# Optimization experiments

Hardware: AMD Instinct MI355X
Metric: run time of the kernel (lower is better)

Reference implementation:

```python
import jax, jax.numpy as jnp
import numpy as np

D_MODEL = 768
NUM_HEADS = 12
SEGMENT_LENGTHS = (2048, 4096, 8192)
DILATION_RATES = (1, 2, 4)
LN_EPS = 1e-5


def setup_inputs() -> dict:
    key = jax.random.key(0)
    ks = jax.random.split(key, 8)
    b, n, dm = 2, 8192, D_MODEL
    s = 1.0 / np.sqrt(dm)
    return {
        "x": jax.random.normal(ks[0], (b, n, dm), dtype=jnp.float32),
        "w_in": jax.random.normal(ks[1], (dm, dm), dtype=jnp.float32) * s,
        "b_in": jnp.zeros((dm,), dtype=jnp.float32),
        "w_out": jax.random.normal(ks[2], (dm, dm), dtype=jnp.float32) * s,
        "b_out": jnp.zeros((dm,), dtype=jnp.float32),
        "ln_gamma": jnp.ones((dm,), dtype=jnp.float32),
        "ln_beta": jnp.zeros((dm,), dtype=jnp.float32),
    }


def _dilated_attention(q, k, v):
    # q, k, v: (b, n, h, d)
    b, n, h, d = q.shape
    num_groups = len(DILATION_RATES)
    group_sizes = [h // num_groups] * num_groups
    for i in range(h % num_groups):
        group_sizes[i] += 1
    scale = 1.0 / jnp.sqrt(jnp.asarray(d, q.dtype))
    out = jnp.zeros_like(q)
    for i, (g, r, s) in enumerate(zip(group_sizes, DILATION_RATES, SEGMENT_LENGTHS)):
        offset = i % r
        hmin, hmax = i * g, (i + 1) * g
        nseg = n // s
        def slc(t):
            # (b, nseg, s, h, d) -> strided dilation slice + head group slice
            return t.reshape(b, nseg, s, h, d)[:, :, offset::r, hmin:hmax, :]
        qs, ks_, vs = slc(q), slc(k), slc(v)  # (b, nseg, se, g, d), se = s // r
        attn = jnp.einsum('bnqhd,bnkhd->bnhqk', qs, ks_) * scale
        attn = jax.nn.softmax(attn, axis=-1)
        x = jnp.einsum('bnhqk,bnkhd->bnqhd', attn, vs)  # (b, nseg, se, g, d)
        # renormalize by sum over (segment, within-segment) dims, as in source
        x = x / x.sum(axis=(1, 2), keepdims=True)
        out = (out.reshape(b, nseg, s, h, d)
                  .at[:, :, offset::r, hmin:hmax, :].add(x)
                  .reshape(b, n, h, d))
    return out / num_groups


def reference(x, w_in, b_in, w_out, b_out, ln_gamma, ln_beta):
    b, n, dm = x.shape
    hd = dm // NUM_HEADS
    # QKVProjectionOption.SAME: q = k = v = proj(x)
    q = x @ w_in.T + b_in
    qh = q.reshape(b, n, NUM_HEADS, hd)
    o = _dilated_attention(qh, qh, qh)
    o = o.reshape(b, n, dm)
    mu = o.mean(axis=-1, keepdims=True)
    var = ((o - mu) ** 2).mean(axis=-1, keepdims=True)
    o = (o - mu) / jnp.sqrt(var + LN_EPS) * ln_gamma + ln_beta
    return o @ w_out.T + b_out
```

## Files before the change

### kernel.cpp

```cpp
#include <hip/hip_runtime.h>
#include <hip/hip_bf16.h>
#include <math.h>

#define B_   2
#define N_   8192
#define DM   768
#define NH   12
#define HD   64

#define QL_ELEM_OFF 12582912ull
#define AC_OFF      12582912ull
#define SUMS_OFF    19922944ull

typedef short bf16x8 __attribute__((ext_vector_type(8)));
typedef _Float16 f16x8 __attribute__((ext_vector_type(8)));
typedef _Float16 f16x4 __attribute__((ext_vector_type(4)));
typedef float f32x4  __attribute__((ext_vector_type(4)));

__device__ __forceinline__ size_t ac_base(int grp) {
    return 8388608ull - (8388608ull >> grp);
}

__device__ __forceinline__ unsigned short f2bf(float f) {
    __hip_bfloat16 h = __float2bfloat16(f);
    return __builtin_bit_cast(unsigned short, h);
}
__device__ __forceinline__ float bf2f(unsigned short u) {
    __hip_bfloat16 h = __builtin_bit_cast(__hip_bfloat16, u);
    return __bfloat162float(h);
}
__device__ __forceinline__ void split2h(float f, _Float16& h, _Float16& l) {
    h = (_Float16)f;
    l = (_Float16)(f - (float)h);
}

#define SW(row, col) ((((row) << 6)) + ((((col) >> 3) ^ ((row) & 7)) << 3) + ((col) & 7))

__global__ __launch_bounds__(256) void gemm_mfma_split(
    const float* __restrict__ A, const float* __restrict__ W,
    const float* __restrict__ bias, float* __restrict__ C,
    _Float16* __restrict__ Ch, _Float16* __restrict__ Cl) {
    __shared__ unsigned short AsH[128][40];
    __shared__ unsigned short AsL[128][40];
    __shared__ unsigned short WsH[128][40];
    __shared__ unsigned short WsL[128][40];

    const int t    = threadIdx.x;
    const int lane = t & 63;
    const int wv   = t >> 6;
    const int c    = lane & 15, q = lane >> 4;
    const int mw   = (wv & 1) * 64, nw = (wv >> 1) * 64;
    const int m0   = blockIdx.x * 128, n0 = blockIdx.y * 128;

    const int srow = t >> 1;
    const int scol = (t & 1) * 16;
    const float* ap = A + (size_t)(m0 + srow) * DM + scol;
    const float* wp = W + (size_t)(n0 + srow) * DM + scol;

    f32x4 acc[4][4];
#pragma unroll
    for (int mi = 0; mi < 4; ++mi)
#pragma unroll
        for (int ni = 0; ni < 4; ++ni) {
            acc[mi][ni][0] = 0.f; acc[mi][ni][1] = 0.f;
            acc[mi][ni][2] = 0.f; acc[mi][ni][3] = 0.f;
        }

    for (int k0 = 0; k0 < DM; k0 += 32) {
        float av[16], wvv[16];
        *(float4*)&av[0]  = *(const float4*)(ap + k0);
        *(float4*)&av[4]  = *(const float4*)(ap + k0 + 4);
        *(float4*)&av[8]  = *(const float4*)(ap + k0 + 8);
        *(float4*)&av[12] = *(const float4*)(ap + k0 + 12);
        *(float4*)&wvv[0]  = *(const float4*)(wp + k0);
        *(float4*)&wvv[4]  = *(const float4*)(wp + k0 + 4);
        *(float4*)&wvv[8]  = *(const float4*)(wp + k0 + 8);
        *(float4*)&wvv[12] = *(const float4*)(wp + k0 + 12);
        __syncthreads();
#pragma unroll
        for (int i = 0; i < 16; ++i) {
            const float x = av[i];
            const unsigned short xh = f2bf(x);
            AsH[srow][scol + i] = xh;
            AsL[srow][scol + i] = f2bf(x - bf2f(xh));
            const float y = wvv[i];
            const unsigned short yh = f2bf(y);
            WsH[srow][scol + i] = yh;
            WsL[srow][scol + i] = f2bf(y - bf2f(yh));
        }
        __syncthreads();

        bf16x8 ah[4], al[4], bh[4], bl[4];
#pragma unroll
        for (int i = 0; i < 4; ++i) {
            ah[i] = *(const bf16x8*)&AsH[mw + i*16 + c][q*8];
            al[i] = *(const bf16x8*)&AsL[mw + i*16 + c][q*8];
            bh[i] = *(const bf16x8*)&WsH[nw + i*16 + c][q*8];
            bl[i] = *(const bf16x8*)&WsL[nw + i*16 + c][q*8];
        }
#pragma unroll
        for (int mi = 0; mi < 4; ++mi)
#pragma unroll
            for (int ni = 0; ni < 4; ++ni) {
                f32x4 v = acc[mi][ni];
                v = __builtin_amdgcn_mfma_f32_16x16x32_bf16(ah[mi], bl[ni], v, 0, 0, 0);
                v = __builtin_amdgcn_mfma_f32_16x16x32_bf16(al[mi], bh[ni], v, 0, 0, 0);
                v = __builtin_amdgcn_mfma_f32_16x16x32_bf16(ah[mi], bh[ni], v, 0, 0, 0);
                acc[mi][ni] = v;
            }
    }

#pragma unroll
    for (int ni = 0; ni < 4; ++ni) {
        const int col = n0 + nw + ni*16 + c;
        const float bv = bias[col];
#pragma unroll
        for (int mi = 0; mi < 4; ++mi)
#pragma unroll
            for (int r = 0; r < 4; ++r) {
                const int row = m0 + mw + mi*16 + q*4 + r;
                const float val = acc[mi][ni][r] + bv;
                if (Ch) {
                    _Float16 hh, ll;
                    split2h(val, hh, ll);
                    Ch[(size_t)row * DM + col] = hh;
                    Cl[(size_t)row * DM + col] = ll;
                } else {
                    C[(size_t)row * DM + col] = val;
                }
            }
    }
}

__global__ __launch_bounds__(256, 3) void attn_mfma_kernel(
    const _Float16* __restrict__ Qh, const _Float16* __restrict__ Ql,
    float* __restrict__ AC) {
    __shared__ __align__(16) _Float16 KH[4096],  KL[4096];
    __shared__ __align__(16) _Float16 VTH[4096], VTL[4096];
    __shared__ __align__(16) _Float16 PTH[4096], PTL[4096];

    const int t    = threadIdx.x;
    const int lane = t & 63;
    const int w    = t >> 6;
    const int c    = lane & 15, quad = lane >> 4;

    const int bi  = blockIdx.x;
    const int qt  = bi & 31;
    const int bsh = bi >> 5;
    int grp, local;
    if (bsh < 32)      { grp = 0; local = bsh; }
    else if (bsh < 48) { grp = 1; local = bsh - 32; }
    else               { grp = 2; local = bsh - 48; }
    const int nseg = 4 >> grp;
    const int sseg = 2048 << grp;
    const int r    = 1 << grp;
    const int b    = local / (nseg * 4);
    const int rem  = local - b * nseg * 4;
    const int seg  = rem >> 2;
    const int hg   = rem & 3;
    const int head = grp * 4 + hg;

    const size_t row0 = (size_t)(b * N_ + seg * sseg + grp);
    const int hoff = head * HD;

    const int r0 = (t >> 4) * 4;
    const int c0 = (t & 15) * 4;

    f16x8 qfh[2], qfl[2];
    {
        const size_t qoff = (row0 + (size_t)(qt*64 + w*16 + c) * r) * DM + hoff;
#pragma unroll
        for (int kc = 0; kc < 2; ++kc) {
            f16x8 h = *(const f16x8*)(Qh + qoff + kc*32 + quad*8);
            f16x8 l = *(const f16x8*)(Ql + qoff + kc*32 + quad*8);
            qfh[kc] = h * (_Float16)0.125f;
            qfl[kc] = l * (_Float16)0.125f;
        }
    }

    {
        f16x4 hh[4], ll[4];
#pragma unroll
        for (int i = 0; i < 4; ++i) {
            const size_t off = (row0 + (size_t)(r0 + i) * r) * DM + hoff + c0;
            hh[i] = *(const f16x4*)(Qh + off);
            ll[i] = *(const f16x4*)(Ql + off);
        }
#pragma unroll
        for (int i = 0; i < 4; ++i) {
            *(f16x4*)&KH[SW(r0 + i, c0)] = hh[i];
            *(f16x4*)&KL[SW(r0 + i, c0)] = ll[i];
        }
#pragma unroll
        for (int j = 0; j < 4; ++j) {
            *(f16x4*)&VTH[SW(c0 + j, r0)] = (f16x4){hh[0][j], hh[1][j], hh[2][j], hh[3][j]};
            *(f16x4*)&VTL[SW(c0 + j, r0)] = (f16x4){ll[0][j], ll[1][j], ll[2][j], ll[3][j]};
        }
    }
    __syncthreads();

    float m_st = -1e30f, l_st = 0.f;
    f32x4 o[4];
#pragma unroll
    for (int i = 0; i < 4; ++i) { o[i][0] = 0.f; o[i][1] = 0.f; o[i][2] = 0.f; o[i][3] = 0.f; }

    for (int kt = 0; kt < 32; ++kt) {
        f16x4 nh[4], nl[4];
        if (kt < 31) {
#pragma unroll
            for (int i = 0; i < 4; ++i) {
                const size_t off = (row0 + (size_t)((kt+1)*64 + r0 + i) * r) * DM + hoff + c0;
                nh[i] = *(const f16x4*)(Qh + off);
                nl[i] = *(const f16x4*)(Ql + off);
            }
        }

        f32x4 s[4];
#pragma unroll
        for (int mt = 0; mt < 4; ++mt) {
            s[mt][0] = 0.f; s[mt][1] = 0.f; s[mt][2] = 0.f; s[mt][3] = 0.f;
        }
#pragma unroll
        for (int kc = 0; kc < 2; ++kc)
#pragma unroll
            for (int mt = 0; mt < 4; ++mt) {
                f16x8 ah = *(const f16x8*)&KH[SW(mt*16 + c, kc*32 + quad*8)];
                f16x8 al = *(const f16x8*)&KL[SW(mt*16 + c, kc*32 + quad*8)];
                f32x4 v = s[mt];
                v = __builtin_amdgcn_mfma_f32_16x16x32_f16(ah, qfl[kc], v, 0, 0, 0);
                v = __builtin_amdgcn_mfma_f32_16x16x32_f16(al, qfh[kc], v, 0, 0, 0);
                v = __builtin_amdgcn_mfma_f32_16x16x32_f16(ah, qfh[kc], v, 0, 0, 0);
                s[mt] = v;
            }

        float mloc = s[0][0];
#pragma unroll
        for (int mt = 0; mt < 4; ++mt)
#pragma unroll
            for (int rg = 0; rg < 4; ++rg) mloc = fmaxf(mloc, s[mt][rg]);
        mloc = fmaxf(mloc, __shfl_xor(mloc, 16));
        mloc = fmaxf(mloc, __shfl_xor(mloc, 32));
        const float mnew  = fmaxf(m_st, mloc);
        const float alpha = __expf(m_st - mnew);
        m_st = mnew;

        float p[16];
        float psum = 0.f;
#pragma unroll
        for (int mt = 0; mt < 4; ++mt)
#pragma unroll
            for (int rg = 0; rg < 4; ++rg) {
                const float pv = __expf(s[mt][rg] - mnew);
                p[mt*4 + rg] = pv;
                psum += pv;
            }
        psum += __shfl_xor(psum, 16);
        psum += __shfl_xor(psum, 32);
        l_st = l_st * alpha + psum;
#pragma unroll
        for (int mtd = 0; mtd < 4; ++mtd) {
            o[mtd][0] *= alpha; o[mtd][1] *= alpha;
            o[mtd][2] *= alpha; o[mtd][3] *= alpha;
        }

#pragma unroll
        for (int mt = 0; mt < 4; ++mt) {
            f16x4 hh, ll;
#pragma unroll
            for (int rg = 0; rg < 4; ++rg) {
                _Float16 th, tl;
                split2h(p[mt*4 + rg], th, tl);
                hh[rg] = th;
                ll[rg] = tl;
            }
            *(f16x4*)&PTH[SW(w*16 + c, mt*16 + quad*4)] = hh;
            *(f16x4*)&PTL[SW(w*16 + c, mt*16 + quad*4)] = ll;
        }

#pragma unroll
        for (int kc = 0; kc < 2; ++kc) {
            f16x8 ph = *(const f16x8*)&PTH[SW(w*16 + c, kc*32 + quad*8)];
            f16x8 pl = *(const f16x8*)&PTL[SW(w*16 + c, kc*32 + quad*8)];
#pragma unroll
            for (int mtd = 0; mtd < 4; ++mtd) {
                f16x8 vh = *(const f16x8*)&VTH[SW(mtd*16 + c, kc*32 + quad*8)];
                f16x8 vl = *(const f16x8*)&VTL[SW(mtd*16 + c, kc*32 + quad*8)];
                f32x4 v = o[mtd];
                v = __builtin_amdgcn_mfma_f32_16x16x32_f16(vh, pl, v, 0, 0, 0);
                v = __builtin_amdgcn_mfma_f32_16x16x32_f16(vl, ph, v, 0, 0, 0);
                v = __builtin_amdgcn_mfma_f32_16x16x32_f16(vh, ph, v, 0, 0, 0);
                o[mtd] = v;
            }
        }

        if (kt < 31) {
            __syncthreads();
#pragma unroll
            for (int i = 0; i < 4; ++i) {
                *(f16x4*)&KH[SW(r0 + i, c0)] = nh[i];
                *(f16x4*)&KL[SW(r0 + i, c0)] = nl[i];
            }
#pragma unroll
            for (int j = 0; j < 4; ++j) {
                *(f16x4*)&VTH[SW(c0 + j, r0)] = (f16x4){nh[0][j], nh[1][j], nh[2][j], nh[3][j]};
                *(f16x4*)&VTL[SW(c0 + j, r0)] = (f16x4){nl[0][j], nl[1][j], nl[2][j], nl[3][j]};
            }
            __syncthreads();
        }
    }

    const size_t gbase = ac_base(grp);
    const float inv = 1.0f / l_st;
    const int qrow = qt*64 + w*16 + c;
    float* dst = AC + gbase + ((size_t)((b*nseg + seg)*2048 + qrow)) * 256 + hg*64;
#pragma unroll
    for (int mtd = 0; mtd < 4; ++mtd) {
        float4 v = make_float4(o[mtd][0]*inv, o[mtd][1]*inv,
                               o[mtd][2]*inv, o[mtd][3]*inv);
        *(float4*)(dst + mtd*16 + quad*4) = v;
    }
}

__global__ __launch_bounds__(256) void sum_kernel(
    const float* __restrict__ AC, float* __restrict__ SUMS) {
    const int bi = blockIdx.x;
    int grp, local;
    if (bi < 64)      { grp = 0; local = bi; }
    else if (bi < 96) { grp = 1; local = bi - 64; }
    else              { grp = 2; local = bi - 96; }
    const int chunks = 32 >> grp;
    const int b  = local / chunks;
    const int ch = local - b * chunks;
    const int P  = 8192 >> grp;
    const size_t base = ac_base(grp) + ((size_t)b * P + ch * 256) * 256 + threadIdx.x;
    float acc = 0.f;
    for (int p = 0; p < 256; ++p) acc += AC[base + (size_t)p * 256];
    atomicAdd(&SUMS[((grp << 1) + b) * 256 + threadIdx.x], acc);
}

__device__ __forceinline__ float block_reduce_sum(float val, float* sdata) {
    __syncthreads();
#pragma unroll
    for (int o = 32; o > 0; o >>= 1) val += __shfl_down(val, o);
    const int lane = threadIdx.x & 63, wid = threadIdx.x >> 6;
    if (lane == 0) sdata[wid] = val;
    __syncthreads();
    return sdata[0] + sdata[1] + sdata[2] + sdata[3];
}

__global__ __launch_bounds__(256) void renorm_ln_kernel(
    const float* __restrict__ AC, const float* __restrict__ SUMS,
    const float* __restrict__ gamma, const float* __restrict__ beta,
    float* __restrict__ OLN) {
    __shared__ float sdata[4];
    const int pos = blockIdx.x;
    const int b = pos >> 13;
    const int n = pos & 8191;

    float v[3];
    int dms[3];
#pragma unroll
    for (int jj = 0; jj < 3; ++jj) {
        const int dm = threadIdx.x + (jj << 8);
        dms[jj] = dm;
        const int h = dm >> 6, d = dm & 63;
        const int grp = h >> 2, hg = h & 3;
        const int r = 1 << grp;
        const int p = n & ((2048 << grp) - 1);
        float val = 0.f;
        if ((p & (r - 1)) == grp) {
            const int nseg = 4 >> grp;
            const int seg  = n >> (11 + grp);
            const int j    = (p - grp) >> grp;
            const float s  = SUMS[((grp << 1) + b) * 256 + (hg << 6) + d];
            val = AC[ac_base(grp) + ((size_t)((b*nseg + seg)*2048 + j)) * 256 + (hg << 6) + d]
                  / (3.0f * s);
        }
        v[jj] = val;
    }

    const float tot = block_reduce_sum(v[0] + v[1] + v[2], sdata);
    const float mu  = tot * (1.0f / 768.0f);
    float sq = 0.f;
#pragma unroll
    for (int jj = 0; jj < 3; ++jj) {
        const float d0 = v[jj] - mu;
        sq += d0 * d0;
    }
    const float var  = block_reduce_sum(sq, sdata) * (1.0f / 768.0f);
    const float rstd = rsqrtf(var + 1e-5f);

    float* dst = OLN + (size_t)pos * 768;
#pragma unroll
    for (int jj = 0; jj < 3; ++jj)
        dst[dms[jj]] = (v[jj] - mu) * rstd * gamma[dms[jj]] + beta[dms[jj]];
}

extern "C" void kernel_launch(void* const* d_in, const int* in_sizes, int n_in,
                              void* d_out, int out_size, void* d_ws, size_t ws_size,
                              hipStream_t stream) {
    const float* x     = (const float*)d_in[0];
    const float* w_in  = (const float*)d_in[1];
    const float* b_in  = (const float*)d_in[2];
    const float* w_out = (const float*)d_in[3];
    const float* b_out = (const float*)d_in[4];
    const float* gamma = (const float*)d_in[5];
    const float* beta  = (const float*)d_in[6];
    float* out = (float*)d_out;

    float* ws   = (float*)d_ws;
    _Float16* Qh = (_Float16*)ws;
    _Float16* Ql = (_Float16*)ws + QL_ELEM_OFF;
    float* AC   = ws + AC_OFF;
    float* SUMS = ws + SUMS_OFF;
    float* OLN  = ws;

    gemm_mfma_split<<<dim3(128, 6), 256, 0, stream>>>(x, w_in, b_in, nullptr, Qh, Ql);
    attn_mfma_kernel<<<1792, 256, 0, stream>>>(Qh, Ql, AC);
    (void)hipMemsetAsync(SUMS, 0, 1536 * sizeof(float), stream);
    sum_kernel<<<112, 256, 0, stream>>>(AC, SUMS);
    renorm_ln_kernel<<<B_ * N_, 256, 0, stream>>>(AC, SUMS, gamma, beta, OLN);
    gemm_mfma_split<<<dim3(128, 6), 256, 0, stream>>>(OLN, w_out, b_out, out,
                                                      nullptr, nullptr);
}
```

Measured before the change: 602.3 us.

## Double query rows per attention block to reuse K/V tiles across two query subtiles

Each attention block now processes 128 query rows instead of 64: every wave handles two 16-row query subtiles, so each K/V tile loaded into shared memory and each K/V fragment read from LDS feeds twice as many MFMAs. The grid is halved to 896 blocks and the P staging buffers are doubled. This cuts global and LDS traffic for K/V per query row. The cost is more registers per thread, with launch bounds lowered from 3 to 2 blocks per SM, and fewer blocks to spread across the GPU.

```diff
diff --git a/kernel.cpp b/kernel.cpp
--- a/kernel.cpp
+++ b/kernel.cpp
@@ -132,12 +132,12 @@
     }
 }
 
-__global__ __launch_bounds__(256, 3) void attn_mfma_kernel(
+__global__ __launch_bounds__(256, 2) void attn_mfma_kernel(
     const _Float16* __restrict__ Qh, const _Float16* __restrict__ Ql,
     float* __restrict__ AC) {
     __shared__ __align__(16) _Float16 KH[4096],  KL[4096];
     __shared__ __align__(16) _Float16 VTH[4096], VTL[4096];
-    __shared__ __align__(16) _Float16 PTH[4096], PTL[4096];
+    __shared__ __align__(16) _Float16 PTH[8192], PTL[8192];
 
     const int t    = threadIdx.x;
     const int lane = t & 63;
@@ -145,8 +145,8 @@
     const int c    = lane & 15, quad = lane >> 4;
 
     const int bi  = blockIdx.x;
-    const int qt  = bi & 31;
-    const int bsh = bi >> 5;
+    const int qt  = bi & 15;
+    const int bsh = bi >> 4;
     int grp, local;
     if (bsh < 32)      { grp = 0; local = bsh; }
     else if (bsh < 48) { grp = 1; local = bsh - 32; }
@@ -166,15 +166,17 @@
     const int r0 = (t >> 4) * 4;
     const int c0 = (t & 15) * 4;
 
-    f16x8 qfh[2], qfl[2];
-    {
-        const size_t qoff = (row0 + (size_t)(qt*64 + w*16 + c) * r) * DM + hoff;
+    f16x8 qfh[2][2], qfl[2][2];
+#pragma unroll
+    for (int jt = 0; jt < 2; ++jt) {
+        const int qrow = qt*128 + w*32 + jt*16 + c;
+        const size_t qoff = (row0 + (size_t)qrow * r) * DM + hoff;
 #pragma unroll
         for (int kc = 0; kc < 2; ++kc) {
             f16x8 h = *(const f16x8*)(Qh + qoff + kc*32 + quad*8);
             f16x8 l = *(const f16x8*)(Ql + qoff + kc*32 + quad*8);
-            qfh[kc] = h * (_Float16)0.125f;
-            qfl[kc] = l * (_Float16)0.125f;
+            qfh[jt][kc] = h * (_Float16)0.125f;
+            qfl[jt][kc] = l * (_Float16)0.125f;
         }
     }
 
@@ -199,10 +201,16 @@
     }
     __syncthreads();
 
-    float m_st = -1e30f, l_st = 0.f;
-    f32x4 o[4];
-#pragma unroll
-    for (int i = 0; i < 4; ++i) { o[i][0] = 0.f; o[i][1] = 0.f; o[i][2] = 0.f; o[i][3] = 0.f; }
+    float m_st[2] = {-1e30f, -1e30f};
+    float l_st[2] = {0.f, 0.f};
+    f32x4 o[2][4];
+#pragma unroll
+    for (int jt = 0; jt < 2; ++jt)
+#pragma unroll
+        for (int i = 0; i < 4; ++i) {
+            o[jt][i][0] = 0.f; o[jt][i][1] = 0.f;
+            o[jt][i][2] = 0.f; o[jt][i][3] = 0.f;
+        }
 
     for (int kt = 0; kt < 32; ++kt) {
         f16x4 nh[4], nl[4];
@@ -215,81 +223,90 @@
             }
         }
 
-        f32x4 s[4];
-#pragma unroll
-        for (int mt = 0; mt < 4; ++mt) {
-            s[mt][0] = 0.f; s[mt][1] = 0.f; s[mt][2] = 0.f; s[mt][3] = 0.f;
-        }
+        f32x4 s[2][4];
+#pragma unroll
+        for (int jt = 0; jt < 2; ++jt)
+#pragma unroll
+            for (int mt = 0; mt < 4; ++mt) {
+                s[jt][mt][0] = 0.f; s[jt][mt][1] = 0.f;
+                s[jt][mt][2] = 0.f; s[jt][mt][3] = 0.f;
+            }
 #pragma unroll
         for (int kc = 0; kc < 2; ++kc)
 #pragma unroll
             for (int mt = 0; mt < 4; ++mt) {
                 f16x8 ah = *(const f16x8*)&KH[SW(mt*16 + c, kc*32 + quad*8)];
                 f16x8 al = *(const f16x8*)&KL[SW(mt*16 + c, kc*32 + quad*8)];
-                f32x4 v = s[mt];
-                v = __builtin_amdgcn_mfma_f32_16x16x32_f16(ah, qfl[kc], v, 0, 0, 0);
-                v = __builtin_amdgcn_mfma_f32_16x16x32_f16(al, qfh[kc], v, 0, 0, 0);
-                v = __builtin_amdgcn_mfma_f32_16x16x32_f16(ah, qfh[kc], v, 0, 0, 0);
-                s[mt] = v;
-            }
-
-        float mloc = s[0][0];
-#pragma unroll
-        for (int mt = 0; mt < 4; ++mt)
-#pragma unroll
-            for (int rg = 0; rg < 4; ++rg) mloc = fmaxf(mloc, s[mt][rg]);
-        mloc = fmaxf(mloc, __shfl_xor(mloc, 16));
-        mloc = fmaxf(mloc, __shfl_xor(mloc, 32));
-        const float mnew  = fmaxf(m_st, mloc);
-        const float alpha = __expf(m_st - mnew);
-        m_st = mnew;
-
-        float p[16];
-        float psum = 0.f;
-#pragma unroll
-        for (int mt = 0; mt < 4; ++mt)
-#pragma unroll
-            for (int rg = 0; rg < 4; ++rg) {
-                const float pv = __expf(s[mt][rg] - mnew);
-                p[mt*4 + rg] = pv;
-                psum += pv;
-            }
-        psum += __shfl_xor(psum, 16);
-        psum += __shfl_xor(psum, 32);
-        l_st = l_st * alpha + psum;
-#pragma unroll
-        for (int mtd = 0; mtd < 4; ++mtd) {
-            o[mtd][0] *= alpha; o[mtd][1] *= alpha;
-            o[mtd][2] *= alpha; o[mtd][3] *= alpha;
-        }
-
-#pragma unroll
-        for (int mt = 0; mt < 4; ++mt) {
-            f16x4 hh, ll;
-#pragma unroll
-            for (int rg = 0; rg < 4; ++rg) {
-                _Float16 th, tl;
-                split2h(p[mt*4 + rg], th, tl);
-                hh[rg] = th;
-                ll[rg] = tl;
-            }
-            *(f16x4*)&PTH[SW(w*16 + c, mt*16 + quad*4)] = hh;
-            *(f16x4*)&PTL[SW(w*16 + c, mt*16 + quad*4)] = ll;
+#pragma unroll
+                for (int jt = 0; jt < 2; ++jt) {
+                    f32x4 v = s[jt][mt];
+                    v = __builtin_amdgcn_mfma_f32_16x16x32_f16(ah, qfl[jt][kc], v, 0, 0, 0);
+                    v = __builtin_amdgcn_mfma_f32_16x16x32_f16(al, qfh[jt][kc], v, 0, 0, 0);
+                    v = __builtin_amdgcn_mfma_f32_16x16x32_f16(ah, qfh[jt][kc], v, 0, 0, 0);
+                    s[jt][mt] = v;
+                }
+            }
+
+#pragma unroll
+        for (int jt = 0; jt < 2; ++jt) {
+            float mloc = s[jt][0][0];
+#pragma unroll
+            for (int mt = 0; mt < 4; ++mt)
+#pragma unroll
+                for (int rg = 0; rg < 4; ++rg) mloc = fmaxf(mloc, s[jt][mt][rg]);
+            mloc = fmaxf(mloc, __shfl_xor(mloc, 16));
+            mloc = fmaxf(mloc, __shfl_xor(mloc, 32));
+            const float mnew  = fmaxf(m_st[jt], mloc);
+            const float alpha = __expf(m_st[jt] - mnew);
+            m_st[jt] = mnew;
+
+            float psum = 0.f;
+            const int prow = w*32 + jt*16 + c;
+#pragma unroll
+            for (int mt = 0; mt < 4; ++mt) {
+                f16x4 hh, ll;
+#pragma unroll
+                for (int rg = 0; rg < 4; ++rg) {
+                    const float pv = __expf(s[jt][mt][rg] - mnew);
+                    psum += pv;
+                    _Float16 th, tl;
+                    split2h(pv, th, tl);
+                    hh[rg] = th;
+                    ll[rg] = tl;
+                }
+                *(f16x4*)&PTH[SW(prow, mt*16 + quad*4)] = hh;
+                *(f16x4*)&PTL[SW(prow, mt*16 + quad*4)] = ll;
+            }
+            psum += __shfl_xor(psum, 16);
+            psum += __shfl_xor(psum, 32);
+            l_st[jt] = l_st[jt] * alpha + psum;
+#pragma unroll
+            for (int mtd = 0; mtd < 4; ++mtd) {
+                o[jt][mtd][0] *= alpha; o[jt][mtd][1] *= alpha;
+                o[jt][mtd][2] *= alpha; o[jt][mtd][3] *= alpha;
+            }
         }
 
 #pragma unroll
         for (int kc = 0; kc < 2; ++kc) {
-            f16x8 ph = *(const f16x8*)&PTH[SW(w*16 + c, kc*32 + quad*8)];
-            f16x8 pl = *(const f16x8*)&PTL[SW(w*16 + c, kc*32 + quad*8)];
+            f16x8 ph[2], pl[2];
+#pragma unroll
+            for (int jt = 0; jt < 2; ++jt) {
+                ph[jt] = *(const f16x8*)&PTH[SW(w*32 + jt*16 + c, kc*32 + quad*8)];
+                pl[jt] = *(const f16x8*)&PTL[SW(w*32 + jt*16 + c, kc*32 + quad*8)];
+            }
 #pragma unroll
             for (int mtd = 0; mtd < 4; ++mtd) {
                 f16x8 vh = *(const f16x8*)&VTH[SW(mtd*16 + c, kc*32 + quad*8)];
                 f16x8 vl = *(const f16x8*)&VTL[SW(mtd*16 + c, kc*32 + quad*8)];
-                f32x4 v = o[mtd];
-                v = __builtin_amdgcn_mfma_f32_16x16x32_f16(vh, pl, v, 0, 0, 0);
-                v = __builtin_amdgcn_mfma_f32_16x16x32_f16(vl, ph, v, 0, 0, 0);
-                v = __builtin_amdgcn_mfma_f32_16x16x32_f16(vh, ph, v, 0, 0, 0);
-                o[mtd] = v;
+#pragma unroll
+                for (int jt = 0; jt < 2; ++jt) {
+                    f32x4 v = o[jt][mtd];
+                    v = __builtin_amdgcn_mfma_f32_16x16x32_f16(vh, pl[jt], v, 0, 0, 0);
+                    v = __builtin_amdgcn_mfma_f32_16x16x32_f16(vl, ph[jt], v, 0, 0, 0);
+                    v = __builtin_amdgcn_mfma_f32_16x16x32_f16(vh, ph[jt], v, 0, 0, 0);
+                    o[jt][mtd] = v;
+                }
             }
         }
 
@@ -310,14 +327,17 @@
     }
 
     const size_t gbase = ac_base(grp);
-    const float inv = 1.0f / l_st;
-    const int qrow = qt*64 + w*16 + c;
-    float* dst = AC + gbase + ((size_t)((b*nseg + seg)*2048 + qrow)) * 256 + hg*64;
-#pragma unroll
-    for (int mtd = 0; mtd < 4; ++mtd) {
-        float4 v = make_float4(o[mtd][0]*inv, o[mtd][1]*inv,
-                               o[mtd][2]*inv, o[mtd][3]*inv);
-        *(float4*)(dst + mtd*16 + quad*4) = v;
+#pragma unroll
+    for (int jt = 0; jt < 2; ++jt) {
+        const float inv = 1.0f / l_st[jt];
+        const int qrow = qt*128 + w*32 + jt*16 + c;
+        float* dst = AC + gbase + ((size_t)((b*nseg + seg)*2048 + qrow)) * 256 + hg*64;
+#pragma unroll
+        for (int mtd = 0; mtd < 4; ++mtd) {
+            float4 v = make_float4(o[jt][mtd][0]*inv, o[jt][mtd][1]*inv,
+                                   o[jt][mtd][2]*inv, o[jt][mtd][3]*inv);
+            *(float4*)(dst + mtd*16 + quad*4) = v;
+        }
     }
 }
 
@@ -416,7 +436,7 @@
     float* OLN  = ws;
 
     gemm_mfma_split<<<dim3(128, 6), 256, 0, stream>>>(x, w_in, b_in, nullptr, Qh, Ql);
-    attn_mfma_kernel<<<1792, 256, 0, stream>>>(Qh, Ql, AC);
+    attn_mfma_kernel<<<896, 256, 0, stream>>>(Qh, Ql, AC);
     (void)hipMemsetAsync(SUMS, 0, 1536 * sizeof(float), stream);
     sum_kernel<<<112, 256, 0, stream>>>(AC, SUMS);
     renorm_ln_kernel<<<B_ * N_, 256, 0, stream>>>(AC, SUMS, gamma, beta, OLN);
```

Measured after the change: 571.2 us. 1.05x faster.
